# Kernel tuning notes

Measured on AMD Instinct MI355X. Metric: run time of the kernel, lower is better.

## Reference

```python
import jax, jax.numpy as jnp
import numpy as np

T, B, D_IN, H = 512, 2048, 128, 16  # seq_len, batch, input_dim, hidden_dim == n_qubits


def _gate(z, theta):
    # Analytic result of the variational circuit:
    # RX(z_i) then RX(theta_i) on |0>, CNOT ladder, PauliZ on every wire
    # => <Z_k> = prod_{j<=k} cos(z_j + theta_j)
    return jnp.cumprod(jnp.cos(z + theta), axis=-1)


def setup_inputs() -> dict:
    key = jax.random.key(0)
    ks = jax.random.split(key, 13)
    fan_in = D_IN + H
    s = 1.0 / np.sqrt(fan_in)
    inputs = jax.random.normal(ks[0], (T, B, D_IN), dtype=jnp.float32)
    def lin(k):
        k1, k2 = jax.random.split(k)
        W = jax.random.uniform(k1, (H, fan_in), jnp.float32, -s, s)
        b = jax.random.uniform(k2, (H,), jnp.float32, -s, s)
        return W, b
    Wf, bf = lin(ks[1]); Wi, bi = lin(ks[2]); Wu, bu = lin(ks[3]); Wo, bo = lin(ks[4])
    theta_f = jax.random.uniform(ks[5], (H,), jnp.float32, 0.0, 2 * np.pi)
    theta_i = jax.random.uniform(ks[6], (H,), jnp.float32, 0.0, 2 * np.pi)
    theta_u = jax.random.uniform(ks[7], (H,), jnp.float32, 0.0, 2 * np.pi)
    theta_o = jax.random.uniform(ks[8], (H,), jnp.float32, 0.0, 2 * np.pi)
    return {"inputs": inputs,
            "Wf": Wf, "bf": bf, "Wi": Wi, "bi": bi,
            "Wu": Wu, "bu": bu, "Wo": Wo, "bo": bo,
            "theta_f": theta_f, "theta_i": theta_i,
            "theta_u": theta_u, "theta_o": theta_o}


def reference(inputs, Wf, bf, Wi, bi, Wu, bu, Wo, bo,
              theta_f, theta_i, theta_u, theta_o):
    Bsz = inputs.shape[1]
    h0 = jnp.zeros((Bsz, H), inputs.dtype)
    c0 = jnp.zeros((Bsz, H), inputs.dtype)

    def step(carry, x_t):
        hx, cx = carry
        comb = jnp.concatenate([x_t, hx], axis=1)          # (B, D_IN+H)
        f = jax.nn.sigmoid(_gate(comb @ Wf.T + bf, theta_f))
        i = jax.nn.sigmoid(_gate(comb @ Wi.T + bi, theta_i))
        g = jnp.tanh(_gate(comb @ Wu.T + bu, theta_u))
        o = jax.nn.sigmoid(_gate(comb @ Wo.T + bo, theta_o))
        cx = f * cx + i * g
        hx = o * jnp.tanh(cx)
        return (hx, cx), hx

    (hx, cx), outputs = jax.lax.scan(step, (h0, c0), inputs)
    return outputs, hx, cx
```

## Files before the change

kernel.cpp:

```cpp
#include <hip/hip_runtime.h>

#define T_STEPS 512
#define BATCH   2048
#define DIN     128
#define NH      16
#define COMB    (DIN + NH)

__device__ __forceinline__ float rcpf(float x)  { return __builtin_amdgcn_rcpf(x); }
__device__ __forceinline__ float sigmf(float x) { return rcpf(1.f + __expf(-x)); }
__device__ __forceinline__ float tanhf_(float x){ float e = __expf(2.f * x); return (e - 1.f) * rcpf(e + 1.f); }

template <int D>
__device__ __forceinline__ float scan_shr(float v) {
    int r = __builtin_amdgcn_update_dpp(0x3f800000, __float_as_int(v),
                                        0x110 | D, 0xF, 0xF, false);
    return __int_as_float(r);
}

__global__ __launch_bounds__(64, 2) void qlstm_kernel(
    const float* __restrict__ x,
    const float* __restrict__ Wf, const float* __restrict__ bf,
    const float* __restrict__ Wi, const float* __restrict__ bi,
    const float* __restrict__ Wu, const float* __restrict__ bu,
    const float* __restrict__ Wo, const float* __restrict__ bo,
    const float* __restrict__ thf, const float* __restrict__ thi,
    const float* __restrict__ thu, const float* __restrict__ tho,
    float* __restrict__ out)
{
    const int lane = threadIdx.x;
    const int k    = lane & 15;
    const int q    = lane >> 4;
    const int b    = blockIdx.x;

    const float* Wg[4] = {Wf, Wi, Wu, Wo};
    const float* bg[4] = {bf, bi, bu, bo};
    const float* tg[4] = {thf, thi, thu, tho};

    float w[4][32], wh[4][4], bt[4];
#pragma unroll
    for (int g = 0; g < 4; ++g) {
        const float* Wr = Wg[g] + k * COMB;
#pragma unroll
        for (int j = 0; j < 32; ++j) w[g][j] = Wr[q * 32 + j];
#pragma unroll
        for (int kk = 0; kk < 4; ++kk) wh[g][kk] = Wr[DIN + q * 4 + kk];
        bt[g] = bg[g][k] + tg[g][k];
    }

    float h = 0.f, c = 0.f;
    float cvA[32], cvB[32];

    auto xrow = [&](int t) -> const float* {
        return x + ((size_t)t * BATCH + b) * DIN + q * 32;
    };
    auto loadx = [&](float (&cv)[32], const float* p) {
#pragma unroll
        for (int j4 = 0; j4 < 8; ++j4) {
            const float4 v = *(const float4*)(p + j4 * 4);
            cv[j4 * 4 + 0] = v.x; cv[j4 * 4 + 1] = v.y;
            cv[j4 * 4 + 2] = v.z; cv[j4 * 4 + 3] = v.w;
        }
    };

    float* op = out + (size_t)b * NH + k;

    auto step = [&](int t, float (&cv)[32]) {
        float acc[4] = {0.f, 0.f, 0.f, 0.f};
#pragma unroll
        for (int j = 0; j < 32; ++j) {
#pragma unroll
            for (int g = 0; g < 4; ++g) acc[g] += cv[j] * w[g][j];
        }
#pragma unroll
        for (int kk = 0; kk < 4; ++kk) {
            const float hv = __shfl(h, q * 4 + kk, 64);
#pragma unroll
            for (int g = 0; g < 4; ++g) acc[g] += hv * wh[g][kk];
        }
#pragma unroll
        for (int g = 0; g < 4; ++g) {
            acc[g] += __shfl_xor(acc[g], 16, 64);
            acc[g] += __shfl_xor(acc[g], 32, 64);
            acc[g] = __cosf(acc[g] + bt[g]);
        }
#pragma unroll
        for (int g = 0; g < 4; ++g) {
            acc[g] *= scan_shr<1>(acc[g]);
            acc[g] *= scan_shr<2>(acc[g]);
            acc[g] *= scan_shr<4>(acc[g]);
            acc[g] *= scan_shr<8>(acc[g]);
        }
        const float f  = sigmf(acc[0]);
        const float i_ = sigmf(acc[1]);
        const float u  = tanhf_(acc[2]);
        const float o  = sigmf(acc[3]);
        c = f * c + i_ * u;
        h = o * tanhf_(c);
        if (q == 0) *op = h;
        op += (size_t)BATCH * NH;
    };

    loadx(cvA, xrow(0));
    for (int t = 0; t < T_STEPS; t += 2) {
        loadx(cvB, xrow(t + 1));
        step(t, cvA);
        const int tn = (t + 2 < T_STEPS) ? t + 2 : T_STEPS - 1;
        loadx(cvA, xrow(tn));
        step(t + 1, cvB);
    }

    if (q == 0) {
        const size_t base = (size_t)T_STEPS * BATCH * NH;
        out[base + (size_t)b * NH + k] = h;
        out[base + (size_t)BATCH * NH + (size_t)b * NH + k] = c;
    }
}

extern "C" void kernel_launch(void* const* d_in, const int* in_sizes, int n_in,
                              void* d_out, int out_size, void* d_ws, size_t ws_size,
                              hipStream_t stream) {
    const float* x   = (const float*)d_in[0];
    const float* Wf  = (const float*)d_in[1];
    const float* bf  = (const float*)d_in[2];
    const float* Wi  = (const float*)d_in[3];
    const float* bi  = (const float*)d_in[4];
    const float* Wu  = (const float*)d_in[5];
    const float* bu  = (const float*)d_in[6];
    const float* Wo  = (const float*)d_in[7];
    const float* bo  = (const float*)d_in[8];
    const float* thf = (const float*)d_in[9];
    const float* thi = (const float*)d_in[10];
    const float* thu = (const float*)d_in[11];
    const float* tho = (const float*)d_in[12];

    qlstm_kernel<<<dim3(BATCH), dim3(64), 0, stream>>>(
        x, Wf, bf, Wi, bi, Wu, bu, Wo, bo, thf, thi, thu, tho, (float*)d_out);
}
```

Measured before the change: 1.169 ms.

## Split input projection into parallel precompute kernel before recurrent scan

Adds a first kernel that computes the input-to-gate projections (x·W plus bias and theta) for all timesteps in parallel and stores them in workspace. A second kernel then runs the recurrence, doing only the small hidden-state matvec, cosine, scan and activations. This takes the large matvec off the serial critical path, at the cost of writing and re-reading a 256 MB (fp32) or 128 MB (bf16) intermediate. The path taken depends on workspace size: fp32, then bf16, then the original monolithic kernel as a fallback.

```diff
diff --git a/kernel.cpp b/kernel.cpp
--- a/kernel.cpp
+++ b/kernel.cpp
@@ -1,10 +1,12 @@
 #include <hip/hip_runtime.h>
+#include <hip/hip_bf16.h>
 
 #define T_STEPS 512
 #define BATCH   2048
 #define DIN     128
 #define NH      16
 #define COMB    (DIN + NH)
+#define ROWS    (T_STEPS * BATCH)
 
 __device__ __forceinline__ float rcpf(float x)  { return __builtin_amdgcn_rcpf(x); }
 __device__ __forceinline__ float sigmf(float x) { return rcpf(1.f + __expf(-x)); }
@@ -17,7 +19,156 @@
     return __int_as_float(r);
 }
 
-__global__ __launch_bounds__(64, 2) void qlstm_kernel(
+__device__ __forceinline__ float zcvt(float v)            { return v; }
+__device__ __forceinline__ float zcvt(__hip_bfloat16 v)   { return __bfloat162float(v); }
+__device__ __forceinline__ void  zstore(float* p, float v){ *p = v; }
+__device__ __forceinline__ void  zstore(__hip_bfloat16* p, float v){ *p = __float2bfloat16(v); }
+
+template <typename ZT>
+__global__ __launch_bounds__(256, 2) void qlstm_phase1(
+    const float* __restrict__ x,
+    const float* __restrict__ Wf, const float* __restrict__ bf,
+    const float* __restrict__ Wi, const float* __restrict__ bi,
+    const float* __restrict__ Wu, const float* __restrict__ bu,
+    const float* __restrict__ Wo, const float* __restrict__ bo,
+    const float* __restrict__ thf, const float* __restrict__ thi,
+    const float* __restrict__ thu, const float* __restrict__ tho,
+    ZT* __restrict__ Zx)
+{
+    const int lane = threadIdx.x & 63;
+    const int k    = lane & 15;
+    const int q    = lane >> 4;
+    const int gw   = blockIdx.x * 4 + (threadIdx.x >> 6);
+    const int NW   = gridDim.x * 4;
+    const int R    = ROWS / NW;
+
+    const float* Wg[4] = {Wf, Wi, Wu, Wo};
+    float w[4][32];
+#pragma unroll
+    for (int g = 0; g < 4; ++g) {
+        const float* Wr = Wg[g] + k * COMB + q * 32;
+#pragma unroll
+        for (int j = 0; j < 32; ++j) w[g][j] = Wr[j];
+    }
+    const float* bgq[4] = {bf, bi, bu, bo};
+    const float* tgq[4] = {thf, thi, thu, tho};
+    const float bt = bgq[q][k] + tgq[q][k];
+
+    const size_t r0 = (size_t)gw * R;
+    const float* xp = x + r0 * DIN + q * 32;
+
+    float cvA[32], cvB[32];
+    auto loadx = [&](float (&cv)[32], int i) {
+        const float* p = xp + (size_t)i * DIN;
+#pragma unroll
+        for (int j4 = 0; j4 < 8; ++j4) {
+            const float4 v = *(const float4*)(p + j4 * 4);
+            cv[j4 * 4 + 0] = v.x; cv[j4 * 4 + 1] = v.y;
+            cv[j4 * 4 + 2] = v.z; cv[j4 * 4 + 3] = v.w;
+        }
+    };
+    auto dorow = [&](int i, float (&cv)[32]) {
+        float acc[4] = {0.f, 0.f, 0.f, 0.f};
+#pragma unroll
+        for (int j = 0; j < 32; ++j)
+#pragma unroll
+            for (int g = 0; g < 4; ++g) acc[g] += cv[j] * w[g][j];
+#pragma unroll
+        for (int g = 0; g < 4; ++g) {
+            acc[g] += __shfl_xor(acc[g], 16, 64);
+            acc[g] += __shfl_xor(acc[g], 32, 64);
+        }
+        const float my = (q == 0) ? acc[0] : (q == 1) ? acc[1]
+                       : (q == 2) ? acc[2] : acc[3];
+        zstore(&Zx[(r0 + i) * 64 + lane], my + bt);
+    };
+
+    loadx(cvA, 0);
+    for (int i = 0; i < R; i += 2) {
+        loadx(cvB, i + 1);
+        dorow(i, cvA);
+        loadx(cvA, i + 2 < R ? i + 2 : R - 1);
+        dorow(i + 1, cvB);
+    }
+}
+
+template <typename ZT>
+__global__ __launch_bounds__(64, 2) void qlstm_phase2(
+    const ZT* __restrict__ Zx,
+    const float* __restrict__ Wf, const float* __restrict__ Wi,
+    const float* __restrict__ Wu, const float* __restrict__ Wo,
+    float* __restrict__ out)
+{
+    const int lane = threadIdx.x;
+    const int k    = lane & 15;
+    const int q    = lane >> 4;
+    const int b    = blockIdx.x;
+
+    const float* Wg[4] = {Wf, Wi, Wu, Wo};
+    float wh[4][4];
+#pragma unroll
+    for (int g = 0; g < 4; ++g)
+#pragma unroll
+        for (int kk = 0; kk < 4; ++kk)
+            wh[g][kk] = Wg[g][k * COMB + DIN + q * 4 + kk];
+
+    float h = 0.f, c = 0.f;
+    float zA[4], zB[4];
+    auto loadz = [&](float (&z)[4], int t) {
+        const ZT* p = Zx + ((size_t)t * BATCH + b) * 64 + k;
+#pragma unroll
+        for (int g = 0; g < 4; ++g) z[g] = zcvt(p[g * 16]);
+    };
+
+    float* op = out + (size_t)b * NH + k;
+
+    auto step = [&](float (&z)[4]) {
+        float acc[4] = {0.f, 0.f, 0.f, 0.f};
+#pragma unroll
+        for (int kk = 0; kk < 4; ++kk) {
+            const float hv = __shfl(h, q * 4 + kk, 64);
+#pragma unroll
+            for (int g = 0; g < 4; ++g) acc[g] += hv * wh[g][kk];
+        }
+#pragma unroll
+        for (int g = 0; g < 4; ++g) {
+            acc[g] += __shfl_xor(acc[g], 16, 64);
+            acc[g] += __shfl_xor(acc[g], 32, 64);
+            acc[g] = __cosf(acc[g] + z[g]);
+        }
+#pragma unroll
+        for (int g = 0; g < 4; ++g) {
+            acc[g] *= scan_shr<1>(acc[g]);
+            acc[g] *= scan_shr<2>(acc[g]);
+            acc[g] *= scan_shr<4>(acc[g]);
+            acc[g] *= scan_shr<8>(acc[g]);
+        }
+        const float f  = sigmf(acc[0]);
+        const float i_ = sigmf(acc[1]);
+        const float u  = tanhf_(acc[2]);
+        const float o  = sigmf(acc[3]);
+        c = f * c + i_ * u;
+        h = o * tanhf_(c);
+        if (q == 0) *op = h;
+        op += (size_t)BATCH * NH;
+    };
+
+    loadz(zA, 0);
+    for (int t = 0; t < T_STEPS; t += 2) {
+        loadz(zB, t + 1);
+        step(zA);
+        loadz(zA, t + 2 < T_STEPS ? t + 2 : T_STEPS - 1);
+        step(zB);
+    }
+
+    if (q == 0) {
+        const size_t base = (size_t)T_STEPS * BATCH * NH;
+        out[base + (size_t)b * NH + k] = h;
+        out[base + (size_t)BATCH * NH + (size_t)b * NH + k] = c;
+    }
+}
+
+__global__ __launch_bounds__(64, 2) void qlstm_mono(
     const float* __restrict__ x,
     const float* __restrict__ Wf, const float* __restrict__ bf,
     const float* __restrict__ Wi, const float* __restrict__ bi,
@@ -49,7 +200,6 @@
 
     float h = 0.f, c = 0.f;
     float cvA[32], cvB[32];
-
     auto xrow = [&](int t) -> const float* {
         return x + ((size_t)t * BATCH + b) * DIN + q * 32;
     };
@@ -63,14 +213,12 @@
     };
 
     float* op = out + (size_t)b * NH + k;
-
     auto step = [&](int t, float (&cv)[32]) {
         float acc[4] = {0.f, 0.f, 0.f, 0.f};
 #pragma unroll
-        for (int j = 0; j < 32; ++j) {
+        for (int j = 0; j < 32; ++j)
 #pragma unroll
             for (int g = 0; g < 4; ++g) acc[g] += cv[j] * w[g][j];
-        }
 #pragma unroll
         for (int kk = 0; kk < 4; ++kk) {
             const float hv = __shfl(h, q * 4 + kk, 64);
@@ -108,7 +256,6 @@
         loadx(cvA, xrow(tn));
         step(t + 1, cvB);
     }
-
     if (q == 0) {
         const size_t base = (size_t)T_STEPS * BATCH * NH;
         out[base + (size_t)b * NH + k] = h;
@@ -132,7 +279,25 @@
     const float* thi = (const float*)d_in[10];
     const float* thu = (const float*)d_in[11];
     const float* tho = (const float*)d_in[12];
-
-    qlstm_kernel<<<dim3(BATCH), dim3(64), 0, stream>>>(
-        x, Wf, bf, Wi, bi, Wu, bu, Wo, bo, thf, thi, thu, tho, (float*)d_out);
-}
+    float* out = (float*)d_out;
+
+    const size_t need_f32  = (size_t)ROWS * 64 * sizeof(float);
+    const size_t need_bf16 = (size_t)ROWS * 64 * sizeof(__hip_bfloat16);
+
+    if (ws_size >= need_f32) {
+        float* Zx = (float*)d_ws;
+        qlstm_phase1<float><<<dim3(2048), dim3(256), 0, stream>>>(
+            x, Wf, bf, Wi, bi, Wu, bu, Wo, bo, thf, thi, thu, tho, Zx);
+        qlstm_phase2<float><<<dim3(BATCH), dim3(64), 0, stream>>>(
+            Zx, Wf, Wi, Wu, Wo, out);
+    } else if (ws_size >= need_bf16) {
+        __hip_bfloat16* Zx = (__hip_bfloat16*)d_ws;
+        qlstm_phase1<__hip_bfloat16><<<dim3(2048), dim3(256), 0, stream>>>(
+            x, Wf, bf, Wi, bi, Wu, bu, Wo, bo, thf, thi, thu, tho, Zx);
+        qlstm_phase2<__hip_bfloat16><<<dim3(BATCH), dim3(64), 0, stream>>>(
+            Zx, Wf, Wi, Wu, Wo, out);
+    } else {
+        qlstm_mono<<<dim3(BATCH), dim3(64), 0, stream>>>(
+            x, Wf, bf, Wi, bi, Wu, bu, Wo, bo, thf, thi, thu, tho, out);
+    }
+}
```

Measured after the change: 1.411 ms. 1.21x slower.
